# Optimization experiments

Hardware: AMD Instinct MI355X
Metric: run time of the kernel (lower is better)

## Reference

```python
import jax, jax.numpy as jnp
import numpy as np

D_MODEL = 1024
NUM_HEADS = 16
HEAD_DIM = D_MODEL // NUM_HEADS
BATCH, SEQ = 2, 2048


def setup_inputs() -> dict:
    key = jax.random.key(0)
    ks = jax.random.split(key, 5)
    scale = 1.0 / np.sqrt(D_MODEL)  # ~xavier magnitude
    x = jax.random.normal(ks[0], (BATCH, SEQ, D_MODEL), dtype=jnp.float32)
    Wq = jax.random.normal(ks[1], (D_MODEL, D_MODEL), dtype=jnp.float32) * scale
    Wk = jax.random.normal(ks[2], (D_MODEL, D_MODEL), dtype=jnp.float32) * scale
    Wv = jax.random.normal(ks[3], (D_MODEL, D_MODEL), dtype=jnp.float32) * scale
    Wo = jax.random.normal(ks[4], (D_MODEL, D_MODEL), dtype=jnp.float32) * scale
    z = jnp.zeros((D_MODEL,), dtype=jnp.float32)
    return {"x": x, "Wq": Wq, "bq": z, "Wk": Wk, "bk": z, "Wv": Wv, "bv": z, "Wo": Wo, "bo": z}


def reference(x, Wq, bq, Wk, bk, Wv, bv, Wo, bo):
    B, S, _ = x.shape
    H, Dh = NUM_HEADS, HEAD_DIM
    # torch Linear convention: y = x @ W^T + b
    q = (x @ Wq.T + bq).reshape(B, S, H, Dh)
    k = (x @ Wk.T + bk).reshape(B, S, H, Dh)
    v = (x @ Wv.T + bv).reshape(B, S, H, Dh)
    # scores: [B, H, S, S]
    scores = jnp.einsum('bqhd,bkhd->bhqk', q, k) / np.sqrt(Dh).astype(np.float32)
    attn = jax.nn.softmax(scores, axis=-1)
    out = jnp.einsum('bhqk,bkhd->bqhd', attn, v).reshape(B, S, H * Dh)
    return out @ Wo.T + bo
```

## Files before the change

### kernel.cpp

```cpp
#include <hip/hip_runtime.h>
#include <hip/hip_bf16.h>

typedef __bf16 bf16;
typedef __bf16 bf16x8 __attribute__((ext_vector_type(8)));
typedef __bf16 bf16x4 __attribute__((ext_vector_type(4)));
typedef float f32x4 __attribute__((ext_vector_type(4)));

constexpr int DM = 1024, NH = 16, DH = 64, NB = 2, SQ = 2048;
constexpr int MTOT = NB * SQ;
constexpr float QSCALE = 0.125f * 1.44269504088896f;

__device__ __forceinline__ void gld_lds16(const bf16* g, bf16* l) {
  __builtin_amdgcn_global_load_lds(
      (const __attribute__((address_space(1))) void*)g,
      (__attribute__((address_space(3))) void*)l, 16, 0, 0);
}

__global__ __launch_bounds__(256) void cvt5(
    const float* __restrict__ s0, const float* __restrict__ s1,
    const float* __restrict__ s2, const float* __restrict__ s3,
    const float* __restrict__ s4,
    bf16* __restrict__ d0, bf16* __restrict__ d1, bf16* __restrict__ d2,
    bf16* __restrict__ d3, bf16* __restrict__ d4) {
  const float* src; bf16* dst; int n;
  switch (blockIdx.y) {
    case 0: src = s0; dst = d0; n = DM * DM; break;
    case 1: src = s1; dst = d1; n = DM * DM; break;
    case 2: src = s2; dst = d2; n = DM * DM; break;
    case 3: src = s3; dst = d3; n = DM * DM; break;
    default: src = s4; dst = d4; n = MTOT * DM; break;
  }
  const int idx = (blockIdx.x * 256 + threadIdx.x) * 4;
  if (idx < n) {
    const float4 v = *(const float4*)(src + idx);
    *(bf16x4*)(dst + idx) = (bf16x4){(bf16)v.x, (bf16)v.y, (bf16)v.z, (bf16)v.w};
  }
}

template <typename OutT>
__device__ __forceinline__ void gemm_tile(
    const bf16* __restrict__ A, const bf16* __restrict__ Bm,
    const float* __restrict__ bias, OutT* __restrict__ C,
    int rowA0, int rowB0, int N, int K, bool bias_row, float cscale,
    bf16* sA, bf16* sB) {
  const int tid = threadIdx.x;
  const int wave = tid >> 6, lane = tid & 63;
  const int wm = wave >> 1, wn = wave & 1;
  const int quad = lane >> 4, l16 = lane & 15;

  f32x4 acc[4][4];
#pragma unroll
  for (int i = 0; i < 4; i++)
#pragma unroll
    for (int j = 0; j < 4; j++) acc[i][j] = (f32x4){0.f, 0.f, 0.f, 0.f};

  const int srow = lane >> 3;
  const int scol = ((lane & 7) ^ srow) * 8;

  auto stage = [&](int kt, int buf) {
#pragma unroll
    for (int i = 0; i < 4; i++) {
      const int r = (wave * 4 + i) * 8;
      gld_lds16(A + (size_t)(rowA0 + r + srow) * K + kt + scol, &sA[buf * 8192 + r * 64]);
      gld_lds16(Bm + (size_t)(rowB0 + r + srow) * K + kt + scol, &sB[buf * 8192 + r * 64]);
    }
  };

  stage(0, 0);
  const int NIT = K / 64;
  for (int it = 0; it < NIT; it++) {
    __syncthreads();
    if (it + 1 < NIT) stage((it + 1) * 64, (it + 1) & 1);
    const bf16* cA = &sA[(it & 1) * 8192];
    const bf16* cB = &sB[(it & 1) * 8192];
#pragma unroll
    for (int kk = 0; kk < 64; kk += 32) {
      bf16x8 aF[4], bF[4];
      const int slot = (((kk >> 3) + quad) ^ (l16 & 7)) << 3;
#pragma unroll
      for (int mt = 0; mt < 4; mt++)
        aF[mt] = *(const bf16x8*)&cA[(wm * 64 + mt * 16 + l16) * 64 + slot];
#pragma unroll
      for (int nt = 0; nt < 4; nt++)
        bF[nt] = *(const bf16x8*)&cB[(wn * 64 + nt * 16 + l16) * 64 + slot];
#pragma unroll
      for (int mt = 0; mt < 4; mt++)
#pragma unroll
        for (int nt = 0; nt < 4; nt++)
          acc[mt][nt] = __builtin_amdgcn_mfma_f32_16x16x32_bf16(aF[mt], bF[nt], acc[mt][nt], 0, 0, 0);
    }
  }

#pragma unroll
  for (int mt = 0; mt < 4; mt++) {
#pragma unroll
    for (int nt = 0; nt < 4; nt++) {
#pragma unroll
      for (int r = 0; r < 4; r++) {
        const int row = rowA0 + wm * 64 + mt * 16 + quad * 4 + r;
        const int col = rowB0 + wn * 64 + nt * 16 + l16;
        const float bb = bias_row ? bias[row] : bias[col];
        C[(size_t)row * N + col] = (OutT)((acc[mt][nt][r] + bb) * cscale);
      }
    }
  }
}

__global__ __launch_bounds__(256, 2) void qkv_gemm(
    const bf16* __restrict__ xb, const bf16* __restrict__ Wqb,
    const bf16* __restrict__ Wkb, const bf16* __restrict__ Wvb,
    const float* __restrict__ bq, const float* __restrict__ bk,
    const float* __restrict__ bv,
    bf16* __restrict__ Qw, bf16* __restrict__ Kw, bf16* __restrict__ VTw) {
  __shared__ alignas(16) bf16 sA[2 * 128 * 64];
  __shared__ alignas(16) bf16 sB[2 * 128 * 64];
  if (blockIdx.z == 0) {
    gemm_tile<bf16>(xb, Wqb, bq, Qw, blockIdx.x * 128, blockIdx.y * 128, DM, DM, false, QSCALE, sA, sB);
  } else if (blockIdx.z == 1) {
    gemm_tile<bf16>(xb, Wkb, bk, Kw, blockIdx.x * 128, blockIdx.y * 128, DM, DM, false, 1.0f, sA, sB);
  } else {
    const int id = blockIdx.y * 32 + blockIdx.x;
    gemm_tile<bf16>(Wvb, xb, bv, VTw, (id >> 5) * 128, (id & 31) * 128, MTOT, DM, true, 1.0f, sA, sB);
  }
}

__global__ __launch_bounds__(256, 2) void out_gemm(
    const bf16* __restrict__ A, const bf16* __restrict__ Bm,
    const float* __restrict__ bias, float* __restrict__ C) {
  __shared__ alignas(16) bf16 sA[2 * 128 * 64];
  __shared__ alignas(16) bf16 sB[2 * 128 * 64];
  gemm_tile<float>(A, Bm, bias, C, blockIdx.x * 128, blockIdx.y * 128, DM, DM, false, 1.0f, sA, sB);
}

__global__ __launch_bounds__(256, 2) void attn(
    const bf16* __restrict__ Q, const bf16* __restrict__ Kq,
    const bf16* __restrict__ VT, bf16* __restrict__ O) {
  __shared__ alignas(16) bf16 sK[2][128 * 64];
  __shared__ alignas(16) bf16 sV[2][64 * 128];
  __shared__ alignas(16) bf16 sP[4][32 * 64];
  const int tid = threadIdx.x, wave = tid >> 6, lane = tid & 63;
  const int quad = lane >> 4, l16 = lane & 15;
  const int hb = blockIdx.x, qt = blockIdx.y;
  const int h = hb & 15, b = hb >> 4;

  const bf16* Qg = Q + (size_t)(b * SQ + qt * 128) * DM + h * DH;
  const bf16* Kg = Kq + (size_t)(b * SQ) * DM + h * DH;
  const bf16* Vg = VT + (size_t)(h * DH) * MTOT + b * SQ;

  const int srow = lane >> 3, scol = ((lane & 7) ^ srow) * 8;
  const int vrow = lane >> 4;

  auto stageKV = [&](int t, int buf) {
#pragma unroll
    for (int i = 0; i < 4; i++) {
      const int r = (wave * 4 + i) * 8;
      gld_lds16(Kg + (size_t)(t * 128 + r + srow) * DM + scol, &sK[buf][r * 64]);
    }
#pragma unroll
    for (int i = 0; i < 4; i++) {
      const int r = (wave * 4 + i) * 4;
      const int vchunk = (lane & 15) ^ ((r + vrow) & 7);
      gld_lds16(Vg + (size_t)(r + vrow) * MTOT + t * 128 + vchunk * 8, &sV[buf][r * 128]);
    }
  };

  bf16x8 qF[2][2];
#pragma unroll
  for (int mt = 0; mt < 2; mt++)
#pragma unroll
    for (int kkh = 0; kkh < 2; kkh++)
      qF[mt][kkh] = *(const bf16x8*)(Qg + (size_t)(wave * 32 + mt * 16 + l16) * DM +
                                     kkh * 32 + quad * 8);

  float l_i[2] = {0.f, 0.f};
  f32x4 o_acc[2][4];
#pragma unroll
  for (int mt = 0; mt < 2; mt++)
#pragma unroll
    for (int n2 = 0; n2 < 4; n2++) o_acc[mt][n2] = (f32x4){0.f, 0.f, 0.f, 0.f};

  stageKV(0, 0);
  for (int t = 0; t < 16; ++t) {
    __syncthreads();
    if (t + 1 < 16) stageKV(t + 1, (t + 1) & 1);
    const bf16* cK = sK[t & 1];
    const bf16* cV = sV[t & 1];

    f32x4 sacc[2][8];
#pragma unroll
    for (int mt = 0; mt < 2; mt++)
#pragma unroll
      for (int nt = 0; nt < 8; nt++) sacc[mt][nt] = (f32x4){0.f, 0.f, 0.f, 0.f};
#pragma unroll
    for (int kk = 0; kk < 64; kk += 32) {
      bf16x8 kF[8];
      const int slot = (((kk >> 3) + quad) ^ (l16 & 7)) << 3;
#pragma unroll
      for (int nt = 0; nt < 8; nt++)
        kF[nt] = *(const bf16x8*)&cK[(nt * 16 + l16) * 64 + slot];
#pragma unroll
      for (int mt = 0; mt < 2; mt++)
#pragma unroll
        for (int nt = 0; nt < 8; nt++)
          sacc[mt][nt] = __builtin_amdgcn_mfma_f32_16x16x32_bf16(kF[nt], qF[mt][kk >> 5],
                                                                 sacc[mt][nt], 0, 0, 0);
    }

#pragma unroll
    for (int half = 0; half < 2; half++) {
#pragma unroll
      for (int mt = 0; mt < 2; mt++) {
        const int row = mt * 16 + l16;
#pragma unroll
        for (int nt4 = 0; nt4 < 4; nt4++) {
          const f32x4 s = sacc[mt][half * 4 + nt4];
          bf16x4 pk;
#pragma unroll
          for (int r = 0; r < 4; r++) {
            const float p = __builtin_amdgcn_exp2f(s[r]);
            l_i[mt] += p;
            pk[r] = (bf16)p;
          }
          const int c = 2 * nt4 + (quad >> 1);
          *(bf16x4*)&sP[wave][row * 64 + ((c ^ (row & 7)) << 3) + (quad & 1) * 4] = pk;
        }
      }
#pragma unroll
      for (int kk = 0; kk < 64; kk += 32) {
        bf16x8 pF[2], vF[4];
#pragma unroll
        for (int mt = 0; mt < 2; mt++) {
          const int row = mt * 16 + l16;
          const int c = (kk >> 3) + quad;
          pF[mt] = *(const bf16x8*)&sP[wave][row * 64 + ((c ^ (row & 7)) << 3)];
        }
#pragma unroll
        for (int n2 = 0; n2 < 4; n2++) {
          const int ch = ((half * 64 + kk) >> 3) + quad;
          vF[n2] = *(const bf16x8*)&cV[(n2 * 16 + l16) * 128 + ((ch ^ (l16 & 7)) << 3)];
        }
#pragma unroll
        for (int mt = 0; mt < 2; mt++)
#pragma unroll
          for (int n2 = 0; n2 < 4; n2++)
            o_acc[mt][n2] = __builtin_amdgcn_mfma_f32_16x16x32_bf16(pF[mt], vF[n2],
                                                                    o_acc[mt][n2], 0, 0, 0);
      }
    }
  }

  float* lbuf = (float*)&sP[wave][0];
#pragma unroll
  for (int mt = 0; mt < 2; mt++) {
    float v = l_i[mt];
    v += __shfl_xor(v, 16);
    v += __shfl_xor(v, 32);
    if (quad == 0) lbuf[mt * 16 + l16] = v;
  }
  __builtin_amdgcn_s_waitcnt(0);
#pragma unroll
  for (int mt = 0; mt < 2; mt++) {
    const f32x4 lv = *(const f32x4*)&lbuf[mt * 16 + quad * 4];
#pragma unroll
    for (int r = 0; r < 4; r++) {
      const float inv = 1.0f / lv[r];
      const int row = qt * 128 + wave * 32 + mt * 16 + quad * 4 + r;
#pragma unroll
      for (int n2 = 0; n2 < 4; n2++) {
        const int col = n2 * 16 + l16;
        O[(size_t)(b * SQ + row) * DM + h * DH + col] = (bf16)(o_acc[mt][n2][r] * inv);
      }
    }
  }
}

extern "C" void kernel_launch(void* const* d_in, const int* in_sizes, int n_in,
                              void* d_out, int out_size, void* d_ws, size_t ws_size,
                              hipStream_t stream) {
  const float* x  = (const float*)d_in[0];
  const float* Wq = (const float*)d_in[1];
  const float* bq = (const float*)d_in[2];
  const float* Wk = (const float*)d_in[3];
  const float* bk = (const float*)d_in[4];
  const float* Wv = (const float*)d_in[5];
  const float* bv = (const float*)d_in[6];
  const float* Wo = (const float*)d_in[7];
  const float* bo = (const float*)d_in[8];
  float* out = (float*)d_out;

  bf16* ws   = (bf16*)d_ws;
  bf16* xb   = ws;
  bf16* Wqb  = ws + (size_t)MTOT * DM;
  bf16* Wkb  = Wqb + (size_t)DM * DM;
  bf16* Wvb  = Wkb + (size_t)DM * DM;
  bf16* Wob  = Wvb + (size_t)DM * DM;
  bf16* Qw   = Wob + (size_t)DM * DM;
  bf16* Kw   = Qw + (size_t)MTOT * DM;
  bf16* VTw  = Kw + (size_t)MTOT * DM;
  bf16* Cw   = VTw + (size_t)MTOT * DM;

  const dim3 blk(256);
  cvt5<<<dim3(MTOT * DM / 1024, 5), blk, 0, stream>>>(Wq, Wk, Wv, Wo, x,
                                                      Wqb, Wkb, Wvb, Wob, xb);
  qkv_gemm<<<dim3(32, 8, 3), blk, 0, stream>>>(xb, Wqb, Wkb, Wvb, bq, bk, bv, Qw, Kw, VTw);
  attn<<<dim3(NH * NB, SQ / 128), blk, 0, stream>>>(Qw, Kw, VTw, Cw);
  out_gemm<<<dim3(MTOT / 128, DM / 128), blk, 0, stream>>>(Cw, Wob, bo, out);
}
```

Baseline: 191.1 us.

## Single-buffer GEMMs for higher occupancy, smaller out-GEMM tiles, MFMA row sums

The shared GEMM tile drops LDS double buffering and syncs twice per k-step. This halves shared memory, so launch bounds rise to 4 blocks per CU. The output projection now uses 64-row tiles, doubling its block count to fill more CUs. The attention kernel computes softmax row sums with an extra MFMA against a ones vector, replacing per-lane scalar adds and a shuffle/LDS reduction. The trade-off is that load latency is no longer overlapped within a block, and the row sum is now taken from bf16-rounded probabilities.

```diff
diff --git a/kernel.cpp b/kernel.cpp
--- a/kernel.cpp
+++ b/kernel.cpp
@@ -37,68 +37,67 @@
   }
 }
 
-template <typename OutT>
+template <int BM, typename OutT>
 __device__ __forceinline__ void gemm_tile(
     const bf16* __restrict__ A, const bf16* __restrict__ Bm,
     const float* __restrict__ bias, OutT* __restrict__ C,
     int rowA0, int rowB0, int N, int K, bool bias_row, float cscale,
     bf16* sA, bf16* sB) {
+  constexpr int NT = (BM == 128) ? 4 : 2;
   const int tid = threadIdx.x;
   const int wave = tid >> 6, lane = tid & 63;
-  const int wm = wave >> 1, wn = wave & 1;
   const int quad = lane >> 4, l16 = lane & 15;
-
-  f32x4 acc[4][4];
+  const int row0w = (BM == 128) ? (wave >> 1) * 64 : 0;
+  const int col0w = (BM == 128) ? (wave & 1) * 64 : wave * 32;
+
+  f32x4 acc[4][NT];
 #pragma unroll
   for (int i = 0; i < 4; i++)
 #pragma unroll
-    for (int j = 0; j < 4; j++) acc[i][j] = (f32x4){0.f, 0.f, 0.f, 0.f};
+    for (int j = 0; j < NT; j++) acc[i][j] = (f32x4){0.f, 0.f, 0.f, 0.f};
 
   const int srow = lane >> 3;
   const int scol = ((lane & 7) ^ srow) * 8;
 
-  auto stage = [&](int kt, int buf) {
+  for (int kt = 0; kt < K; kt += 64) {
+#pragma unroll
+    for (int i = 0; i < BM / 32; i++) {
+      const int r = i * 32 + wave * 8;
+      gld_lds16(A + (size_t)(rowA0 + r + srow) * K + kt + scol, &sA[r * 64]);
+    }
 #pragma unroll
     for (int i = 0; i < 4; i++) {
-      const int r = (wave * 4 + i) * 8;
-      gld_lds16(A + (size_t)(rowA0 + r + srow) * K + kt + scol, &sA[buf * 8192 + r * 64]);
-      gld_lds16(Bm + (size_t)(rowB0 + r + srow) * K + kt + scol, &sB[buf * 8192 + r * 64]);
-    }
-  };
-
-  stage(0, 0);
-  const int NIT = K / 64;
-  for (int it = 0; it < NIT; it++) {
+      const int r = i * 32 + wave * 8;
+      gld_lds16(Bm + (size_t)(rowB0 + r + srow) * K + kt + scol, &sB[r * 64]);
+    }
     __syncthreads();
-    if (it + 1 < NIT) stage((it + 1) * 64, (it + 1) & 1);
-    const bf16* cA = &sA[(it & 1) * 8192];
-    const bf16* cB = &sB[(it & 1) * 8192];
 #pragma unroll
     for (int kk = 0; kk < 64; kk += 32) {
-      bf16x8 aF[4], bF[4];
+      bf16x8 aF[4], bF[NT];
       const int slot = (((kk >> 3) + quad) ^ (l16 & 7)) << 3;
 #pragma unroll
       for (int mt = 0; mt < 4; mt++)
-        aF[mt] = *(const bf16x8*)&cA[(wm * 64 + mt * 16 + l16) * 64 + slot];
-#pragma unroll
-      for (int nt = 0; nt < 4; nt++)
-        bF[nt] = *(const bf16x8*)&cB[(wn * 64 + nt * 16 + l16) * 64 + slot];
+        aF[mt] = *(const bf16x8*)&sA[(row0w + mt * 16 + l16) * 64 + slot];
+#pragma unroll
+      for (int nt = 0; nt < NT; nt++)
+        bF[nt] = *(const bf16x8*)&sB[(col0w + nt * 16 + l16) * 64 + slot];
 #pragma unroll
       for (int mt = 0; mt < 4; mt++)
 #pragma unroll
-        for (int nt = 0; nt < 4; nt++)
+        for (int nt = 0; nt < NT; nt++)
           acc[mt][nt] = __builtin_amdgcn_mfma_f32_16x16x32_bf16(aF[mt], bF[nt], acc[mt][nt], 0, 0, 0);
     }
+    __syncthreads();
   }
 
 #pragma unroll
   for (int mt = 0; mt < 4; mt++) {
 #pragma unroll
-    for (int nt = 0; nt < 4; nt++) {
+    for (int nt = 0; nt < NT; nt++) {
 #pragma unroll
       for (int r = 0; r < 4; r++) {
-        const int row = rowA0 + wm * 64 + mt * 16 + quad * 4 + r;
-        const int col = rowB0 + wn * 64 + nt * 16 + l16;
+        const int row = rowA0 + row0w + mt * 16 + quad * 4 + r;
+        const int col = rowB0 + col0w + nt * 16 + l16;
         const float bb = bias_row ? bias[row] : bias[col];
         C[(size_t)row * N + col] = (OutT)((acc[mt][nt][r] + bb) * cscale);
       }
@@ -106,30 +105,30 @@
   }
 }
 
-__global__ __launch_bounds__(256, 2) void qkv_gemm(
+__global__ __launch_bounds__(256, 4) void qkv_gemm(
     const bf16* __restrict__ xb, const bf16* __restrict__ Wqb,
     const bf16* __restrict__ Wkb, const bf16* __restrict__ Wvb,
     const float* __restrict__ bq, const float* __restrict__ bk,
     const float* __restrict__ bv,
     bf16* __restrict__ Qw, bf16* __restrict__ Kw, bf16* __restrict__ VTw) {
-  __shared__ alignas(16) bf16 sA[2 * 128 * 64];
-  __shared__ alignas(16) bf16 sB[2 * 128 * 64];
+  __shared__ alignas(16) bf16 sA[128 * 64];
+  __shared__ alignas(16) bf16 sB[128 * 64];
   if (blockIdx.z == 0) {
-    gemm_tile<bf16>(xb, Wqb, bq, Qw, blockIdx.x * 128, blockIdx.y * 128, DM, DM, false, QSCALE, sA, sB);
+    gemm_tile<128, bf16>(xb, Wqb, bq, Qw, blockIdx.x * 128, blockIdx.y * 128, DM, DM, false, QSCALE, sA, sB);
   } else if (blockIdx.z == 1) {
-    gemm_tile<bf16>(xb, Wkb, bk, Kw, blockIdx.x * 128, blockIdx.y * 128, DM, DM, false, 1.0f, sA, sB);
+    gemm_tile<128, bf16>(xb, Wkb, bk, Kw, blockIdx.x * 128, blockIdx.y * 128, DM, DM, false, 1.0f, sA, sB);
   } else {
     const int id = blockIdx.y * 32 + blockIdx.x;
-    gemm_tile<bf16>(Wvb, xb, bv, VTw, (id >> 5) * 128, (id & 31) * 128, MTOT, DM, true, 1.0f, sA, sB);
-  }
-}
-
-__global__ __launch_bounds__(256, 2) void out_gemm(
+    gemm_tile<128, bf16>(Wvb, xb, bv, VTw, (id >> 5) * 128, (id & 31) * 128, MTOT, DM, true, 1.0f, sA, sB);
+  }
+}
+
+__global__ __launch_bounds__(256, 4) void out_gemm(
     const bf16* __restrict__ A, const bf16* __restrict__ Bm,
     const float* __restrict__ bias, float* __restrict__ C) {
-  __shared__ alignas(16) bf16 sA[2 * 128 * 64];
-  __shared__ alignas(16) bf16 sB[2 * 128 * 64];
-  gemm_tile<float>(A, Bm, bias, C, blockIdx.x * 128, blockIdx.y * 128, DM, DM, false, 1.0f, sA, sB);
+  __shared__ alignas(16) bf16 sA[64 * 64];
+  __shared__ alignas(16) bf16 sB[128 * 64];
+  gemm_tile<64, float>(A, Bm, bias, C, blockIdx.x * 64, blockIdx.y * 128, DM, DM, false, 1.0f, sA, sB);
 }
 
 __global__ __launch_bounds__(256, 2) void attn(
@@ -172,12 +171,18 @@
       qF[mt][kkh] = *(const bf16x8*)(Qg + (size_t)(wave * 32 + mt * 16 + l16) * DM +
                                      kkh * 32 + quad * 8);
 
-  float l_i[2] = {0.f, 0.f};
+  bf16x8 onesF;
+#pragma unroll
+  for (int i = 0; i < 8; i++) onesF[i] = (bf16)1.0f;
+
+  f32x4 l_acc[2];
   f32x4 o_acc[2][4];
 #pragma unroll
-  for (int mt = 0; mt < 2; mt++)
+  for (int mt = 0; mt < 2; mt++) {
+    l_acc[mt] = (f32x4){0.f, 0.f, 0.f, 0.f};
 #pragma unroll
     for (int n2 = 0; n2 < 4; n2++) o_acc[mt][n2] = (f32x4){0.f, 0.f, 0.f, 0.f};
+  }
 
   stageKV(0, 0);
   for (int t = 0; t < 16; ++t) {
@@ -216,11 +221,7 @@
           const f32x4 s = sacc[mt][half * 4 + nt4];
           bf16x4 pk;
 #pragma unroll
-          for (int r = 0; r < 4; r++) {
-            const float p = __builtin_amdgcn_exp2f(s[r]);
-            l_i[mt] += p;
-            pk[r] = (bf16)p;
-          }
+          for (int r = 0; r < 4; r++) pk[r] = (bf16)__builtin_amdgcn_exp2f(s[r]);
           const int c = 2 * nt4 + (quad >> 1);
           *(bf16x4*)&sP[wave][row * 64 + ((c ^ (row & 7)) << 3) + (quad & 1) * 4] = pk;
         }
@@ -240,30 +241,22 @@
           vF[n2] = *(const bf16x8*)&cV[(n2 * 16 + l16) * 128 + ((ch ^ (l16 & 7)) << 3)];
         }
 #pragma unroll
-        for (int mt = 0; mt < 2; mt++)
+        for (int mt = 0; mt < 2; mt++) {
 #pragma unroll
           for (int n2 = 0; n2 < 4; n2++)
             o_acc[mt][n2] = __builtin_amdgcn_mfma_f32_16x16x32_bf16(pF[mt], vF[n2],
                                                                     o_acc[mt][n2], 0, 0, 0);
+          l_acc[mt] = __builtin_amdgcn_mfma_f32_16x16x32_bf16(pF[mt], onesF, l_acc[mt], 0, 0, 0);
+        }
       }
     }
   }
 
-  float* lbuf = (float*)&sP[wave][0];
 #pragma unroll
   for (int mt = 0; mt < 2; mt++) {
-    float v = l_i[mt];
-    v += __shfl_xor(v, 16);
-    v += __shfl_xor(v, 32);
-    if (quad == 0) lbuf[mt * 16 + l16] = v;
-  }
-  __builtin_amdgcn_s_waitcnt(0);
-#pragma unroll
-  for (int mt = 0; mt < 2; mt++) {
-    const f32x4 lv = *(const f32x4*)&lbuf[mt * 16 + quad * 4];
 #pragma unroll
     for (int r = 0; r < 4; r++) {
-      const float inv = 1.0f / lv[r];
+      const float inv = 1.0f / l_acc[mt][r];
       const int row = qt * 128 + wave * 32 + mt * 16 + quad * 4 + r;
 #pragma unroll
       for (int n2 = 0; n2 < 4; n2++) {
@@ -304,5 +297,5 @@
                                                       Wqb, Wkb, Wvb, Wob, xb);
   qkv_gemm<<<dim3(32, 8, 3), blk, 0, stream>>>(xb, Wqb, Wkb, Wvb, bq, bk, bv, Qw, Kw, VTw);
   attn<<<dim3(NH * NB, SQ / 128), blk, 0, stream>>>(Qw, Kw, VTw, Cw);
-  out_gemm<<<dim3(MTOT / 128, DM / 128), blk, 0, stream>>>(Cw, Wob, bo, out);
-}
+  out_gemm<<<dim3(MTOT / 64, DM / 128), blk, 0, stream>>>(Cw, Wob, bo, out);
+}
```

New measurement: 178.5 us. 1.07x faster.
